# Kernel tuning notes

Measured on AMD Instinct MI355X. Metric: run time of the kernel, lower is better.

## Reference

```python
import jax, jax.numpy as jnp
import numpy as np

H = 512  # hidden_dim

def setup_inputs() -> dict:
    key = jax.random.key(0)
    k1, k2, k3, k4, k5 = jax.random.split(key, 5)
    B, S = 32, 2048
    hidden = jax.random.normal(k1, (B, 2 * H), dtype=jnp.float32)
    encoder_outputs = jax.random.normal(k2, (B, S, 2 * H), dtype=jnp.float32)
    # nn.Linear(4H, H): weight [H, 4H], bias [H]
    W = jax.random.normal(k3, (H, 4 * H), dtype=jnp.float32) / np.sqrt(4 * H)
    b = jnp.zeros((H,), dtype=jnp.float32)
    v = jax.random.normal(k4, (H,), dtype=jnp.float32) / np.sqrt(H)
    return {"hidden": hidden, "encoder_outputs": encoder_outputs, "W": W, "b": b, "v": v}

def reference(hidden, encoder_outputs, W, b, v):
    B, S, _ = encoder_outputs.shape
    # concat repeated decoder hidden with encoder outputs: [B, S, 4H]
    hidden_rep = jnp.broadcast_to(hidden[:, None, :], (B, S, hidden.shape[-1]))
    cat = jnp.concatenate([hidden_rep, encoder_outputs], axis=-1)
    energy = jnp.tanh(jnp.einsum('bsf,hf->bsh', cat, W) + b)  # [B, S, H]
    scores = jnp.einsum('bsh,h->bs', energy, v)               # [B, S]
    attn = jax.nn.softmax(scores, axis=1)                     # softmax over seq
    context = jnp.einsum('bsd,bs->bd', encoder_outputs, attn) # [B, 2H]
    return context
```

## Files before the change

kernel.cpp:

```cpp
#include <hip/hip_runtime.h>


typedef __fp16   half2v __attribute__((ext_vector_type(2)));
typedef _Float16 half8  __attribute__((ext_vector_type(8)));
typedef __attribute__((ext_vector_type(4)))  float f4;
typedef __attribute__((ext_vector_type(16))) float f16v;
typedef __attribute__((ext_vector_type(4)))  unsigned int uint4v;

__device__ __forceinline__ void gload_lds16(const void* g, void* l) {
    __builtin_amdgcn_global_load_lds(
        (const __attribute__((address_space(1))) unsigned int*)g,
        (__attribute__((address_space(3))) unsigned int*)l, 16, 0, 0);
}
__device__ __forceinline__ unsigned int bc2(half2v h) {
    return __builtin_bit_cast(unsigned int, h);
}
#define MEMPIN asm volatile("" ::: "memory")

__global__ __launch_bounds__(256) void prep_kernel(
    const float* __restrict__ hidden, const float* __restrict__ W,
    const float* __restrict__ bias, float* __restrict__ u,
    unsigned short* __restrict__ w2) {
    __shared__ float hid_s[1024];
    if (blockIdx.x < 256) {
        int g = blockIdx.x * 256 + threadIdx.x;
        int kk = g >> 11, id = g & 2047;
        int ntg = id >> 7, kh = (id >> 6) & 1, l = id & 63;
        int h = (ntg << 5) + (l & 31);
        int kg = 1024 + (kk << 5) + (kh << 4) + ((l >> 5) << 3);
        const float* src = W + (size_t)h * 2048 + kg;
        f4 x0 = *(const f4*)src;
        f4 x1 = *(const f4*)(src + 4);
        half8 vh;
        #pragma unroll
        for (int j = 0; j < 4; ++j) vh[j] = (_Float16)x0[j];
        #pragma unroll
        for (int j = 0; j < 4; ++j) vh[4 + j] = (_Float16)x1[j];
        ((half8*)w2)[g] = vh;
    } else {
        const int t = threadIdx.x;
        const int blk = (int)blockIdx.x - 256;
        const int b = blk >> 3, hg = blk & 7;
        ((f4*)hid_s)[t] = ((const f4*)(hidden + ((size_t)b << 10)))[t];
        __syncthreads();
        const int w = t >> 6, lane = t & 63;
        const f4* hid4 = (const f4*)hid_s;
        #pragma unroll 2
        for (int i = 0; i < 16; ++i) {
            int h = (hg << 6) + (w << 4) + i;
            const f4* wr = (const f4*)(W + (size_t)h * 2048);
            float p = 0.f;
            #pragma unroll
            for (int i2 = 0; i2 < 4; ++i2) {
                f4 w4 = wr[lane + (i2 << 6)];
                f4 h4 = hid4[lane + (i2 << 6)];
                p += w4[0]*h4[0] + w4[1]*h4[1] + w4[2]*h4[2] + w4[3]*h4[3];
            }
            #pragma unroll
            for (int off = 1; off < 64; off <<= 1) p += __shfl_xor(p, off);
            if (lane == 0) u[((size_t)b << 9) + h] = bias[h] + p;
        }
    }
}

__global__ __launch_bounds__(256, 3) void score_kernel(
    const float* __restrict__ enc, const unsigned short* __restrict__ w2,
    const float* __restrict__ u, const float* __restrict__ v,
    float* __restrict__ scores_part) {
    __shared__ short Ahi[2][2048], Alo[2][2048];
    __shared__ short Bs[2][8192];
    __shared__ float u_s[256], v_s[256];
    __shared__ float partial[4][64];

    const int tid  = threadIdx.x;
    const int wl   = tid >> 6, lane = tid & 63;
    const int col  = lane & 31;
    const int sblk = blockIdx.x >> 1, hh = blockIdx.x & 1;
    const int row0 = sblk * 64;
    const int b    = row0 >> 11;
    const float* encB = enc + (size_t)row0 * 1024;

    u_s[tid] = u[(b << 9) + (hh << 8) + tid];
    v_s[tid] = v[(hh << 8) + tid];

    f16v acc[2][2];
    #pragma unroll
    for (int mt = 0; mt < 2; ++mt)
        #pragma unroll
        for (int nt = 0; nt < 2; ++nt)
            #pragma unroll
            for (int r = 0; r < 16; ++r) acc[mt][nt][r] = 0.f;

    const int s_mt = tid >> 7, s_kh = (tid >> 6) & 1, s_l = tid & 63;
    const int s_row = (s_mt << 5) + (s_l & 31);
    const int s_kb  = (s_kh << 4) + ((s_l >> 5) << 3);
    const float* aSrc = encB + (size_t)s_row * 1024 + s_kb;

#define STAGE_B(buf, kkex) do {                                               \
        const char* bsrc_ = (const char*)w2 + (size_t)(kkex) * 32768          \
                            + (hh << 14) + (wl << 12) + lane * 16;            \
        char* bdst_ = (char*)(&Bs[buf][0]) + (wl << 12);                      \
        gload_lds16(bsrc_,        bdst_);                                     \
        gload_lds16(bsrc_ + 1024, bdst_ + 1024);                              \
        gload_lds16(bsrc_ + 2048, bdst_ + 2048);                              \
        gload_lds16(bsrc_ + 3072, bdst_ + 3072);                              \
    } while (0)

#define CVT_WRITE_A(buf, r0, r1) do {                                         \
        half2v h01 = __builtin_amdgcn_cvt_pkrtz(r0[0], r0[1]);                \
        half2v h23 = __builtin_amdgcn_cvt_pkrtz(r0[2], r0[3]);                \
        half2v h45 = __builtin_amdgcn_cvt_pkrtz(r1[0], r1[1]);                \
        half2v h67 = __builtin_amdgcn_cvt_pkrtz(r1[2], r1[3]);                \
        half2v l01 = __builtin_amdgcn_cvt_pkrtz(r0[0] - (float)h01[0], r0[1] - (float)h01[1]); \
        half2v l23 = __builtin_amdgcn_cvt_pkrtz(r0[2] - (float)h23[0], r0[3] - (float)h23[1]); \
        half2v l45 = __builtin_amdgcn_cvt_pkrtz(r1[0] - (float)h45[0], r1[1] - (float)h45[1]); \
        half2v l67 = __builtin_amdgcn_cvt_pkrtz(r1[2] - (float)h67[0], r1[3] - (float)h67[1]); \
        uint4v hp_ = {bc2(h01), bc2(h23), bc2(h45), bc2(h67)};                \
        uint4v lp_ = {bc2(l01), bc2(l23), bc2(l45), bc2(l67)};                \
        ((uint4v*)(&Ahi[buf][0]))[tid] = hp_;                                 \
        ((uint4v*)(&Alo[buf][0]))[tid] = lp_;                                 \
    } while (0)

#define COMPUTE(buf) do {                                                     \
        const half8* Ah8_ = (const half8*)(&Ahi[buf][0]);                     \
        const half8* Al8_ = (const half8*)(&Alo[buf][0]);                     \
        const half8* Bh8_ = (const half8*)(&Bs[buf][0]);                      \
        __builtin_amdgcn_s_setprio(1);                                        \
        _Pragma("unroll")                                                     \
        for (int kh = 0; kh < 2; ++kh) {                                      \
            half8 ah0 = Ah8_[(kh << 6) + lane];                               \
            half8 ah1 = Ah8_[128 + (kh << 6) + lane];                         \
            half8 al0 = Al8_[(kh << 6) + lane];                               \
            half8 al1 = Al8_[128 + (kh << 6) + lane];                         \
            _Pragma("unroll")                                                 \
            for (int nt = 0; nt < 2; ++nt) {                                  \
                int ntl = (wl << 1) + nt;                                     \
                half8 b8 = Bh8_[((ntl << 1) + kh) * 64 + lane];               \
                acc[0][nt] = __builtin_amdgcn_mfma_f32_32x32x16_f16(ah0, b8, acc[0][nt], 0, 0, 0); \
                acc[0][nt] = __builtin_amdgcn_mfma_f32_32x32x16_f16(al0, b8, acc[0][nt], 0, 0, 0); \
                acc[1][nt] = __builtin_amdgcn_mfma_f32_32x32x16_f16(ah1, b8, acc[1][nt], 0, 0, 0); \
                acc[1][nt] = __builtin_amdgcn_mfma_f32_32x32x16_f16(al1, b8, acc[1][nt], 0, 0, 0); \
            }                                                                 \
        }                                                                     \
        __builtin_amdgcn_s_setprio(0);                                        \
    } while (0)

#define ITER(kkex, curlit, cx0, cx1, lx0, lx1) do {                           \
        STAGE_B(curlit ^ 1, (kkex) + 1);                                      \
        MEMPIN;                                                               \
        int kc_ = (kkex) + 2; if (kc_ > 31) kc_ = 31;                         \
        lx0 = *(const f4*)(aSrc + (kc_ << 5));                                \
        lx1 = *(const f4*)(aSrc + (kc_ << 5) + 4);                            \
        MEMPIN;                                                               \
        COMPUTE(curlit);                                                      \
        asm volatile("s_waitcnt vmcnt(6)" ::: "memory");                      \
        CVT_WRITE_A(curlit ^ 1, cx0, cx1);                                    \
        asm volatile("s_waitcnt vmcnt(2) lgkmcnt(0)" ::: "memory");           \
        __builtin_amdgcn_s_barrier();                                         \
        __builtin_amdgcn_sched_barrier(0);                                    \
    } while (0)

    f4 xa0, xa1, xb0, xb1;
    {
        f4 z0 = *(const f4*)(aSrc);
        f4 z1 = *(const f4*)(aSrc + 4);
        MEMPIN;
        STAGE_B(0, 0);
        MEMPIN;
        xa0 = *(const f4*)(aSrc + 32);
        xa1 = *(const f4*)(aSrc + 36);
        MEMPIN;
        CVT_WRITE_A(0, z0, z1);
        asm volatile("s_waitcnt vmcnt(2) lgkmcnt(0)" ::: "memory");
        __builtin_amdgcn_s_barrier();
        __builtin_amdgcn_sched_barrier(0);
    }

    #pragma unroll 1
    for (int kk = 0; kk < 30; kk += 2) {
        ITER(kk,     0, xa0, xa1, xb0, xb1);
        ITER(kk + 1, 1, xb0, xb1, xa0, xa1);
    }
    ITER(30, 0, xa0, xa1, xb0, xb1);
    COMPUTE(1);

#undef ITER
#undef COMPUTE
#undef CVT_WRITE_A
#undef STAGE_B

    const int rhalf = (lane >> 5) << 2;
    #pragma unroll
    for (int mt = 0; mt < 2; ++mt) {
        #pragma unroll
        for (int reg = 0; reg < 16; ++reg) {
            float ssum = 0.f;
            #pragma unroll
            for (int nt = 0; nt < 2; ++nt) {
                int hl = (((wl << 1) + nt) << 5) + col;
                float x = u_s[hl] + acc[mt][nt][reg];
                float t = __expf(2.f * x);
                float th = 1.f - 2.f / (t + 1.f);
                ssum += v_s[hl] * th;
            }
            ssum += __shfl_xor(ssum, 1);
            ssum += __shfl_xor(ssum, 2);
            ssum += __shfl_xor(ssum, 4);
            ssum += __shfl_xor(ssum, 8);
            ssum += __shfl_xor(ssum, 16);
            if (col == 0)
                partial[wl][(mt << 5) + (reg & 3) + ((reg >> 2) << 3) + rhalf] = ssum;
        }
    }
    __syncthreads();
    if (tid < 64) {
        float s = partial[0][tid] + partial[1][tid] + partial[2][tid] + partial[3][tid];
        scores_part[(hh << 16) + row0 + tid] = s;
    }
}

__global__ __launch_bounds__(256) void ctx_partial_kernel(
    const float* __restrict__ enc, const float* __restrict__ scores_part,
    float* __restrict__ partials) {
    __shared__ float p_s[2048];
    __shared__ float wredm[4], wreds[4];
    const int t = threadIdx.x;
    const int b = blockIdx.x >> 5, sc = blockIdx.x & 31;
    const int wid = t >> 6, lane = t & 63;
    const float* s0 = scores_part + ((size_t)b << 11);
    const float* s1 = s0 + 65536;

    float vals[8];
    float mx = -1e30f;
    #pragma unroll
    for (int i = 0; i < 8; ++i) {
        int idx = t + (i << 8);
        vals[i] = s0[idx] + s1[idx];
        mx = fmaxf(mx, vals[i]);
    }
    #pragma unroll
    for (int off = 1; off < 64; off <<= 1) mx = fmaxf(mx, __shfl_xor(mx, off));
    if (lane == 0) wredm[wid] = mx;
    __syncthreads();
    mx = fmaxf(fmaxf(wredm[0], wredm[1]), fmaxf(wredm[2], wredm[3]));

    float lsum = 0.f;
    #pragma unroll
    for (int i = 0; i < 8; ++i) {
        float e = __expf(vals[i] - mx);
        p_s[t + (i << 8)] = e;
        lsum += e;
    }
    #pragma unroll
    for (int off = 1; off < 64; off <<= 1) lsum += __shfl_xor(lsum, off);
    if (lane == 0) wreds[wid] = lsum;
    __syncthreads();
    const float inv = 1.f / (wreds[0] + wreds[1] + wreds[2] + wreds[3]);

    f4 a0 = (f4){0.f, 0.f, 0.f, 0.f};
    f4 a1 = (f4){0.f, 0.f, 0.f, 0.f};
    const f4* erow = ((const f4*)(enc + ((size_t)b * 2048 + (sc << 6)) * 1024)) + t;
    #pragma unroll 8
    for (int i = 0; i < 64; i += 2) {
        a0 += p_s[(sc << 6) + i]     * erow[(size_t)i << 8];
        a1 += p_s[(sc << 6) + i + 1] * erow[((size_t)(i + 1)) << 8];
    }
    f4 a = (a0 + a1) * inv;
    f4* dst = (f4*)(partials + (((size_t)(sc << 5) + b) << 10));
    dst[t] = a;
}

__global__ __launch_bounds__(256) void ctx_reduce_kernel(
    const float* __restrict__ partials, float* __restrict__ out) {
    int i = blockIdx.x * 256 + threadIdx.x;
    float s = 0.f;
    #pragma unroll
    for (int sc = 0; sc < 32; ++sc) s += partials[sc * 32768 + i];
    out[i] = s;
}

extern "C" void kernel_launch(void* const* d_in, const int* in_sizes, int n_in,
                              void* d_out, int out_size, void* d_ws, size_t ws_size,
                              hipStream_t stream) {
    const float* hidden = (const float*)d_in[0];
    const float* enc    = (const float*)d_in[1];
    const float* W      = (const float*)d_in[2];
    const float* bias   = (const float*)d_in[3];
    const float* v      = (const float*)d_in[4];
    float* out = (float*)d_out;
    char* ws = (char*)d_ws;

    float* u            = (float*)(ws);
    float* scores_part  = (float*)(ws + 65536);
    float* partials     = (float*)(ws + 589824);
    unsigned short* w2  = (unsigned short*)(ws + 4784128);

    prep_kernel<<<512, 256, 0, stream>>>(hidden, W, bias, u, w2);
    score_kernel<<<2048, 256, 0, stream>>>(enc, w2, u, v, scores_part);
    ctx_partial_kernel<<<1024, 256, 0, stream>>>(enc, scores_part, partials);
    ctx_reduce_kernel<<<128, 256, 0, stream>>>(partials, out);
}
```

Baseline: 547.9 us.

## Single-buffer score GEMM LDS and split softmax into separate kernel

Measured after the change: 520.2 us. 5.1% less time.

```diff
diff --git a/kernel.cpp b/kernel.cpp
--- a/kernel.cpp
+++ b/kernel.cpp
@@ -67,8 +67,8 @@
     const float* __restrict__ enc, const unsigned short* __restrict__ w2,
     const float* __restrict__ u, const float* __restrict__ v,
     float* __restrict__ scores_part) {
-    __shared__ short Ahi[2][2048], Alo[2][2048];
-    __shared__ short Bs[2][8192];
+    __shared__ short Ahi[2048], Alo[2048];
+    __shared__ short Bs[8192];
     __shared__ float u_s[256], v_s[256];
     __shared__ float partial[4][64];
 
@@ -96,17 +96,22 @@
     const int s_kb  = (s_kh << 4) + ((s_l >> 5) << 3);
     const float* aSrc = encB + (size_t)s_row * 1024 + s_kb;
 
-#define STAGE_B(buf, kkex) do {                                               \
-        const char* bsrc_ = (const char*)w2 + (size_t)(kkex) * 32768          \
-                            + (hh << 14) + (wl << 12) + lane * 16;            \
-        char* bdst_ = (char*)(&Bs[buf][0]) + (wl << 12);                      \
-        gload_lds16(bsrc_,        bdst_);                                     \
-        gload_lds16(bsrc_ + 1024, bdst_ + 1024);                              \
-        gload_lds16(bsrc_ + 2048, bdst_ + 2048);                              \
-        gload_lds16(bsrc_ + 3072, bdst_ + 3072);                              \
+    const char* bBase = (const char*)w2 + (hh << 14) + (wl << 12) + lane * 16;
+    char* bdst = (char*)Bs + (wl << 12);
+
+    const half8* Ah8 = (const half8*)Ahi;
+    const half8* Al8 = (const half8*)Alo;
+    const half8* Bh8 = (const half8*)Bs;
+
+#define STAGE_B(kkex) do {                                                    \
+        const char* bs_ = bBase + (size_t)(kkex) * 32768;                     \
+        gload_lds16(bs_,        bdst);                                        \
+        gload_lds16(bs_ + 1024, bdst + 1024);                                 \
+        gload_lds16(bs_ + 2048, bdst + 2048);                                 \
+        gload_lds16(bs_ + 3072, bdst + 3072);                                 \
     } while (0)
 
-#define CVT_WRITE_A(buf, r0, r1) do {                                         \
+#define CVT_WRITE_A(r0, r1) do {                                              \
         half2v h01 = __builtin_amdgcn_cvt_pkrtz(r0[0], r0[1]);                \
         half2v h23 = __builtin_amdgcn_cvt_pkrtz(r0[2], r0[3]);                \
         half2v h45 = __builtin_amdgcn_cvt_pkrtz(r1[0], r1[1]);                \
@@ -117,72 +122,54 @@
         half2v l67 = __builtin_amdgcn_cvt_pkrtz(r1[2] - (float)h67[0], r1[3] - (float)h67[1]); \
         uint4v hp_ = {bc2(h01), bc2(h23), bc2(h45), bc2(h67)};                \
         uint4v lp_ = {bc2(l01), bc2(l23), bc2(l45), bc2(l67)};                \
-        ((uint4v*)(&Ahi[buf][0]))[tid] = hp_;                                 \
-        ((uint4v*)(&Alo[buf][0]))[tid] = lp_;                                 \
+        ((uint4v*)Ahi)[tid] = hp_;                                            \
+        ((uint4v*)Alo)[tid] = lp_;                                            \
     } while (0)
 
-#define COMPUTE(buf) do {                                                     \
-        const half8* Ah8_ = (const half8*)(&Ahi[buf][0]);                     \
-        const half8* Al8_ = (const half8*)(&Alo[buf][0]);                     \
-        const half8* Bh8_ = (const half8*)(&Bs[buf][0]);                      \
-        __builtin_amdgcn_s_setprio(1);                                        \
+#define COMPUTE() do {                                                        \
         _Pragma("unroll")                                                     \
         for (int kh = 0; kh < 2; ++kh) {                                      \
-            half8 ah0 = Ah8_[(kh << 6) + lane];                               \
-            half8 ah1 = Ah8_[128 + (kh << 6) + lane];                         \
-            half8 al0 = Al8_[(kh << 6) + lane];                               \
-            half8 al1 = Al8_[128 + (kh << 6) + lane];                         \
+            half8 ah0 = Ah8[(kh << 6) + lane];                                \
+            half8 ah1 = Ah8[128 + (kh << 6) + lane];                          \
+            half8 al0 = Al8[(kh << 6) + lane];                                \
+            half8 al1 = Al8[128 + (kh << 6) + lane];                          \
             _Pragma("unroll")                                                 \
             for (int nt = 0; nt < 2; ++nt) {                                  \
                 int ntl = (wl << 1) + nt;                                     \
-                half8 b8 = Bh8_[((ntl << 1) + kh) * 64 + lane];               \
+                half8 b8 = Bh8[((ntl << 1) + kh) * 64 + lane];                \
                 acc[0][nt] = __builtin_amdgcn_mfma_f32_32x32x16_f16(ah0, b8, acc[0][nt], 0, 0, 0); \
                 acc[0][nt] = __builtin_amdgcn_mfma_f32_32x32x16_f16(al0, b8, acc[0][nt], 0, 0, 0); \
                 acc[1][nt] = __builtin_amdgcn_mfma_f32_32x32x16_f16(ah1, b8, acc[1][nt], 0, 0, 0); \
                 acc[1][nt] = __builtin_amdgcn_mfma_f32_32x32x16_f16(al1, b8, acc[1][nt], 0, 0, 0); \
             }                                                                 \
         }                                                                     \
-        __builtin_amdgcn_s_setprio(0);                                        \
     } while (0)
 
-#define ITER(kkex, curlit, cx0, cx1, lx0, lx1) do {                           \
-        STAGE_B(curlit ^ 1, (kkex) + 1);                                      \
+#define ITER(kkex, cx0, cx1, lx0, lx1) do {                                   \
+        __builtin_amdgcn_s_barrier();                                         \
+        STAGE_B(kkex);                                                        \
         MEMPIN;                                                               \
-        int kc_ = (kkex) + 2; if (kc_ > 31) kc_ = 31;                         \
-        lx0 = *(const f4*)(aSrc + (kc_ << 5));                                \
-        lx1 = *(const f4*)(aSrc + (kc_ << 5) + 4);                            \
+        int kn_ = (kkex) + 1; if (kn_ > 31) kn_ = 31;                         \
+        lx0 = *(const f4*)(aSrc + (kn_ << 5));                                \
+        lx1 = *(const f4*)(aSrc + (kn_ << 5) + 4);                            \
         MEMPIN;                                                               \
-        COMPUTE(curlit);                                                      \
-        asm volatile("s_waitcnt vmcnt(6)" ::: "memory");                      \
-        CVT_WRITE_A(curlit ^ 1, cx0, cx1);                                    \
+        CVT_WRITE_A(cx0, cx1);                                                \
         asm volatile("s_waitcnt vmcnt(2) lgkmcnt(0)" ::: "memory");           \
         __builtin_amdgcn_s_barrier();                                         \
         __builtin_amdgcn_sched_barrier(0);                                    \
+        COMPUTE();                                                            \
     } while (0)
 
-    f4 xa0, xa1, xb0, xb1;
-    {
-        f4 z0 = *(const f4*)(aSrc);
-        f4 z1 = *(const f4*)(aSrc + 4);
-        MEMPIN;
-        STAGE_B(0, 0);
-        MEMPIN;
-        xa0 = *(const f4*)(aSrc + 32);
-        xa1 = *(const f4*)(aSrc + 36);
-        MEMPIN;
-        CVT_WRITE_A(0, z0, z1);
-        asm volatile("s_waitcnt vmcnt(2) lgkmcnt(0)" ::: "memory");
-        __builtin_amdgcn_s_barrier();
-        __builtin_amdgcn_sched_barrier(0);
-    }
+    f4 xa0 = *(const f4*)(aSrc);
+    f4 xa1 = *(const f4*)(aSrc + 4);
+    f4 xb0, xb1;
+    asm volatile("s_waitcnt lgkmcnt(0)" ::: "memory");
 
     #pragma unroll 1
-    for (int kk = 0; kk < 30; kk += 2) {
-        ITER(kk,     0, xa0, xa1, xb0, xb1);
-        ITER(kk + 1, 1, xb0, xb1, xa0, xa1);
-    }
-    ITER(30, 0, xa0, xa1, xb0, xb1);
-    COMPUTE(1);
+    for (int kk = 0; kk < 32; kk += 2) {
+        ITER(kk,     xa0, xa1, xb0, xb1);
+        ITER(kk + 1, xb0, xb1, xa0, xa1);
+    }
 
 #undef ITER
 #undef COMPUTE
@@ -219,15 +206,11 @@
     }
 }
 
-__global__ __launch_bounds__(256) void ctx_partial_kernel(
-    const float* __restrict__ enc, const float* __restrict__ scores_part,
-    float* __restrict__ partials) {
-    __shared__ float p_s[2048];
+__global__ __launch_bounds__(256) void softmax_kernel(float* scores_part) {
     __shared__ float wredm[4], wreds[4];
-    const int t = threadIdx.x;
-    const int b = blockIdx.x >> 5, sc = blockIdx.x & 31;
+    const int t = threadIdx.x, b = blockIdx.x;
     const int wid = t >> 6, lane = t & 63;
-    const float* s0 = scores_part + ((size_t)b << 11);
+    float* s0 = scores_part + ((size_t)b << 11);
     const float* s1 = s0 + 65536;
 
     float vals[8];
@@ -244,28 +227,43 @@
     __syncthreads();
     mx = fmaxf(fmaxf(wredm[0], wredm[1]), fmaxf(wredm[2], wredm[3]));
 
-    float lsum = 0.f;
+    float e[8], lsum = 0.f;
     #pragma unroll
     for (int i = 0; i < 8; ++i) {
-        float e = __expf(vals[i] - mx);
-        p_s[t + (i << 8)] = e;
-        lsum += e;
+        e[i] = __expf(vals[i] - mx);
+        lsum += e[i];
     }
     #pragma unroll
     for (int off = 1; off < 64; off <<= 1) lsum += __shfl_xor(lsum, off);
     if (lane == 0) wreds[wid] = lsum;
     __syncthreads();
     const float inv = 1.f / (wreds[0] + wreds[1] + wreds[2] + wreds[3]);
+    #pragma unroll
+    for (int i = 0; i < 8; ++i) s0[t + (i << 8)] = e[i] * inv;
+}
+
+__global__ __launch_bounds__(256) void ctx_partial_kernel(
+    const float* __restrict__ enc, const float* __restrict__ attn,
+    float* __restrict__ partials) {
+    __shared__ float a_s[64];
+    const int t = threadIdx.x;
+    const int b = blockIdx.x >> 5, sc = blockIdx.x & 31;
+    if (t < 64) a_s[t] = attn[((size_t)b << 11) + (sc << 6) + t];
+    __syncthreads();
 
     f4 a0 = (f4){0.f, 0.f, 0.f, 0.f};
     f4 a1 = (f4){0.f, 0.f, 0.f, 0.f};
+    f4 a2 = (f4){0.f, 0.f, 0.f, 0.f};
+    f4 a3 = (f4){0.f, 0.f, 0.f, 0.f};
     const f4* erow = ((const f4*)(enc + ((size_t)b * 2048 + (sc << 6)) * 1024)) + t;
-    #pragma unroll 8
-    for (int i = 0; i < 64; i += 2) {
-        a0 += p_s[(sc << 6) + i]     * erow[(size_t)i << 8];
-        a1 += p_s[(sc << 6) + i + 1] * erow[((size_t)(i + 1)) << 8];
-    }
-    f4 a = (a0 + a1) * inv;
+    #pragma unroll 4
+    for (int i = 0; i < 64; i += 4) {
+        a0 += a_s[i]     * erow[(size_t)i << 8];
+        a1 += a_s[i + 1] * erow[((size_t)(i + 1)) << 8];
+        a2 += a_s[i + 2] * erow[((size_t)(i + 2)) << 8];
+        a3 += a_s[i + 3] * erow[((size_t)(i + 3)) << 8];
+    }
+    f4 a = (a0 + a1) + (a2 + a3);
     f4* dst = (f4*)(partials + (((size_t)(sc << 5) + b) << 10));
     dst[t] = a;
 }
@@ -297,6 +295,7 @@
 
     prep_kernel<<<512, 256, 0, stream>>>(hidden, W, bias, u, w2);
     score_kernel<<<2048, 256, 0, stream>>>(enc, w2, u, v, scores_part);
+    softmax_kernel<<<32, 256, 0, stream>>>(scores_part);
     ctx_partial_kernel<<<1024, 256, 0, stream>>>(enc, scores_part, partials);
     ctx_reduce_kernel<<<128, 256, 0, stream>>>(partials, out);
 }
```
